# Optimization experiments

Hardware: AMD Instinct MI355X
Metric: run time of the kernel (lower is better)

The kernel has to match this reference:

```python
import jax, jax.numpy as jnp
import numpy as np

KERNEL_MUL = 2.0
KERNEL_NUM = 5
ZERO_SUM_FILL = 100.0  # original replaces zero class-sums with 100 before dividing


def _cal_weight(s_label, t_label):
    # s_label, t_label: [B, C]; normalize each class column by its batch mass,
    # zero out classes absent in either domain (faithful to intended semantics).
    s_sum = jnp.sum(s_label, axis=0, keepdims=True)           # [1, C]
    t_sum = jnp.sum(t_label, axis=0, keepdims=True)           # [1, C]
    s_vec = s_label / jnp.where(s_sum == 0, ZERO_SUM_FILL, s_sum)
    t_vec = t_label / jnp.where(t_sum == 0, ZERO_SUM_FILL, t_sum)
    valid = ((s_sum != 0) & (t_sum != 0)).astype(s_label.dtype)  # [1, C]
    s_vec = s_vec * valid
    t_vec = t_vec * valid
    w_ss = s_vec @ s_vec.T   # [B, B]
    w_tt = t_vec @ t_vec.T   # [B, B]
    w_st = s_vec @ t_vec.T   # [B, B]
    return w_ss, w_tt, w_st


def _multi_kernel(source, target):
    n = source.shape[0] + target.shape[0]
    total = jnp.concatenate([source, target], axis=0)          # [N, D]
    # pairwise squared L2 via GEMM trick: same math as (x_i - x_j)^2 summed over D
    sq = jnp.sum(total * total, axis=1)                        # [N]
    l2 = sq[:, None] + sq[None, :] - 2.0 * (total @ total.T)   # [N, N]
    # bandwidth from detached distances (median-like heuristic)
    bw = jax.lax.stop_gradient(jnp.sum(l2)) / (n * n - n)
    bw = bw / (KERNEL_MUL ** (KERNEL_NUM // 2))
    kernels = jnp.zeros_like(l2)
    for i in range(KERNEL_NUM):
        kernels = kernels + jnp.exp(-l2 / (bw * (KERNEL_MUL ** i)))
    return kernels


def setup_inputs() -> dict:
    key = jax.random.key(0)
    k1, k2, k3, k4 = jax.random.split(key, 4)
    B, D, C = 4096, 256, 31
    return {
        "source": jax.random.normal(k1, (B, D), dtype=jnp.float32),
        "target": jax.random.normal(k2, (B, D), dtype=jnp.float32),
        "s_label": jax.random.uniform(k3, (B, C), dtype=jnp.float32),
        "t_label": jax.random.uniform(k4, (B, C), dtype=jnp.float32),
    }


def reference(source, target, s_label, t_label):
    B = source.shape[0]
    # weights are computed in numpy in the original -> constants w.r.t. grads
    w_ss, w_tt, w_st = _cal_weight(jax.lax.stop_gradient(s_label),
                                   jax.lax.stop_gradient(t_label))
    kernels = _multi_kernel(source, target)                    # [2B, 2B]
    SS = kernels[:B, :B]
    TT = kernels[B:, B:]
    ST = kernels[:B, B:]
    loss = jnp.sum(w_ss * SS + w_tt * TT - 2.0 * w_st * ST)
    return loss.reshape(1)
```

## Files before the change

### kernel.cpp

```cpp
#include <hip/hip_runtime.h>
#include <hip/hip_bf16.h>
#include <math.h>

#define BN 4096
#define DD 256
#define CC 31
#define KP 352
#define AUGA 256
#define AUGB 288
#define LABK 320

typedef __attribute__((ext_vector_type(8))) short bf16x8;
typedef __attribute__((ext_vector_type(4))) float f32x4;

static __device__ inline unsigned short f2bf(float v) {
  __hip_bfloat16 h = __float2bfloat16(v);
  union { __hip_bfloat16 h; unsigned short u; } cv;
  cv.h = h;
  return cv.u;
}
static __device__ inline float bf2f(unsigned short u) {
  return __uint_as_float(((unsigned int)u) << 16);
}


__global__ void colscale_kernel(const float* __restrict__ s_label,
                                const float* __restrict__ t_label,
                                float* __restrict__ aScale,
                                float* __restrict__ bScale) {
  int c = blockIdx.x;
  int t = threadIdx.x;
  double ss = 0.0, ts = 0.0;
  if (c < CC) {
    for (int r = t; r < BN; r += 256) {
      ss += (double)s_label[(size_t)r * CC + c];
      ts += (double)t_label[(size_t)r * CC + c];
    }
  }
  for (int off = 32; off; off >>= 1) {
    ss += __shfl_xor(ss, off);
    ts += __shfl_xor(ts, off);
  }
  __shared__ double rS[4], rT[4];
  int w = t >> 6, lane = t & 63;
  if (lane == 0) { rS[w] = ss; rT[w] = ts; }
  __syncthreads();
  if (t == 0) {
    double s_sum = rS[0] + rS[1] + rS[2] + rS[3];
    double t_sum = rT[0] + rT[1] + rT[2] + rT[3];
    bool valid = (c < CC) && (s_sum != 0.0) && (t_sum != 0.0);
    aScale[c] = valid ? (float)(1.0 / s_sum) : 0.f;
    bScale[c] = valid ? (float)(1.0 / t_sum) : 0.f;
  }
}

__global__ void stats_kernel(const float* __restrict__ source,
                             const float* __restrict__ target,
                             double* __restrict__ colsum,
                             double* __restrict__ sumsq) {
  const int d = threadIdx.x;
  const int r0 = blockIdx.x * 32;
  float cs = 0.f, sq = 0.f;
  for (int r = r0; r < r0 + 32; ++r) {
    const float v = (r < BN) ? source[(size_t)r * DD + d]
                             : target[(size_t)(r - BN) * DD + d];
    cs += v;
    sq += v * v;
  }
  atomicAdd(&colsum[d], (double)cs);
  __shared__ float red[256];
  red[d] = sq;
  __syncthreads();
  for (int s = 128; s; s >>= 1) {
    if (d < s) red[d] += red[d + s];
    __syncthreads();
  }
  if (d == 0) atomicAdd(sumsq, (double)red[0]);
}

__global__ void bw_kernel(const double* __restrict__ sumsq,
                          const double* __restrict__ colsum,
                          float* __restrict__ negc) {
  __shared__ double red[256];
  int t = threadIdx.x;
  double cs = colsum[t];
  red[t] = cs * cs;
  __syncthreads();
  for (int s = 128; s; s >>= 1) {
    if (t < s) red[t] += red[t + s];
    __syncthreads();
  }
  if (t == 0) {
    double suml2 = 2.0 * 8192.0 * (*sumsq) - 2.0 * red[0];
    double bw = suml2 / (8192.0 * 8192.0 - 8192.0);
    bw = bw / 4.0;
    for (int k = 0; k < 5; ++k)
      negc[k] = (float)(-1.0 / (bw * (double)(1 << k)));
  }
}

__global__ void pack_kernel(const float* __restrict__ source,
                            const float* __restrict__ target,
                            const float* __restrict__ s_label,
                            const float* __restrict__ t_label,
                            const float* __restrict__ aScale,
                            const float* __restrict__ bScale,
                            unsigned short* __restrict__ pack) {
  const int vr = blockIdx.x;
  const int l = threadIdx.x;
  const bool isS = (vr < BN);
  const float* xp = isS ? (source + (size_t)vr * DD)
                        : (target + (size_t)(vr - BN) * DD);
  float4 v = ((const float4*)xp)[l];
  unsigned short ub[4] = {f2bf(v.x), f2bf(v.y), f2bf(v.z), f2bf(v.w)};
  float f[4];
#pragma unroll
  for (int e = 0; e < 4; ++e) f[e] = bf2f(ub[e]);
  float sq = f[0] * f[0] + f[1] * f[1] + f[2] * f[2] + f[3] * f[3];
#pragma unroll
  for (int off = 32; off; off >>= 1) sq += __shfl_xor(sq, off);

  const size_t rb = (size_t)vr * KP;
  *(short4*)&pack[rb + l * 4] =
      make_short4((short)ub[0], (short)ub[1], (short)ub[2], (short)ub[3]);

  if (l < 8) {
    const unsigned short one = f2bf(1.0f);
    const float hs = -0.5f * sq;
    const unsigned short hh = f2bf(hs);
    const unsigned short lo = f2bf(hs - bf2f(hh));
    const int c0 = l * 4;
    unsigned short a_aug[4], b_aug[4], labv[4];
#pragma unroll
    for (int e = 0; e < 4; ++e) {
      const int c = c0 + e;
      a_aug[e] = (c == 0) ? hh : (c == 1) ? lo : (c <= 3) ? one : (unsigned short)0;
      b_aug[e] = (c <= 1) ? one : (c == 2) ? hh : (c == 3) ? lo : (unsigned short)0;
      float lv = 0.f;
      if (c < CC) {
        lv = isS ? s_label[(size_t)vr * CC + c] * aScale[c]
                 : t_label[(size_t)(vr - BN) * CC + c] * bScale[c];
      }
      labv[e] = f2bf(lv);
    }
    *(short4*)&pack[rb + AUGA + c0] = make_short4(
        (short)a_aug[0], (short)a_aug[1], (short)a_aug[2], (short)a_aug[3]);
    *(short4*)&pack[rb + AUGB + c0] = make_short4(
        (short)b_aug[0], (short)b_aug[1], (short)b_aug[2], (short)b_aug[3]);
    *(short4*)&pack[rb + LABK + c0] = make_short4(
        (short)labv[0], (short)labv[1], (short)labv[2], (short)labv[3]);
  }
}

__global__ __launch_bounds__(256) void lmmd_main(
    const unsigned short* __restrict__ pack, const float* __restrict__ negc,
    double* __restrict__ accOut) {
  __shared__ __align__(16) unsigned short bufB[2][128][32];
  __shared__ double dred[256];

  const int t = threadIdx.x;
  const int lane = t & 63;
  const int wv = t >> 6;
  const int bi = blockIdx.x >> 6;
  const int bj = blockIdx.x & 63;
  const int r15 = lane & 15;
  const int kb0 = (lane >> 4) * 8;

  const int rowSi = (bi * 64 + wv * 16 + r15) * KP;
  const int rowTi = rowSi + BN * KP;

  const int srow = t >> 1;
  const int soff = (t & 1) * 16;
  const int srowG = (srow < 64) ? (bj * 64 + srow) : (BN + bj * 64 + (srow - 64));
  const size_t sbase = (size_t)srowG * KP;

  constexpr int koAarr[10] = {0, 32, 64, 96, 128, 160, 192, 224, AUGA, LABK};
  constexpr int koBarr[10] = {0, 32, 64, 96, 128, 160, 192, 224, AUGB, LABK};

  f32x4 aSS[4], aTT[4], aST[4], wSS[4], wTT[4], wST[4];
#pragma unroll
  for (int n = 0; n < 4; ++n) {
    aSS[n] = {0.f, 0.f, 0.f, 0.f};
    aTT[n] = {0.f, 0.f, 0.f, 0.f};
    aST[n] = {0.f, 0.f, 0.f, 0.f};
    wSS[n] = {0.f, 0.f, 0.f, 0.f};
    wTT[n] = {0.f, 0.f, 0.f, 0.f};
    wST[n] = {0.f, 0.f, 0.f, 0.f};
  }

  {
    const float4 v0 = *(const float4*)&pack[sbase + koBarr[0] + soff];
    const float4 v1 = *(const float4*)&pack[sbase + koBarr[0] + soff + 8];
    *(float4*)&bufB[0][srow][soff] = v0;
    *(float4*)&bufB[0][srow][soff + 8] = v1;
  }

#pragma unroll
  for (int c = 0; c < 10; ++c) {
    __syncthreads();
    float4 s0, s1;
    if (c < 9) {
      s0 = *(const float4*)&pack[sbase + koBarr[c + 1] + soff];
      s1 = *(const float4*)&pack[sbase + koBarr[c + 1] + soff + 8];
    }
    const bf16x8 aS = *(const bf16x8*)&pack[rowSi + koAarr[c] + kb0];
    const bf16x8 aT = *(const bf16x8*)&pack[rowTi + koAarr[c] + kb0];
    const int cb = c & 1;
#pragma unroll
    for (int n = 0; n < 4; ++n) {
      const bf16x8 bS = *(const bf16x8*)&bufB[cb][n * 16 + r15][kb0];
      const bf16x8 bT = *(const bf16x8*)&bufB[cb][64 + n * 16 + r15][kb0];
      if (c < 9) {
        aSS[n] = __builtin_amdgcn_mfma_f32_16x16x32_bf16(aS, bS, aSS[n], 0, 0, 0);
        aTT[n] = __builtin_amdgcn_mfma_f32_16x16x32_bf16(aT, bT, aTT[n], 0, 0, 0);
        aST[n] = __builtin_amdgcn_mfma_f32_16x16x32_bf16(aS, bT, aST[n], 0, 0, 0);
      } else {
        wSS[n] = __builtin_amdgcn_mfma_f32_16x16x32_bf16(aS, bS, wSS[n], 0, 0, 0);
        wTT[n] = __builtin_amdgcn_mfma_f32_16x16x32_bf16(aT, bT, wTT[n], 0, 0, 0);
        wST[n] = __builtin_amdgcn_mfma_f32_16x16x32_bf16(aS, bT, wST[n], 0, 0, 0);
      }
    }
    if (c < 9) {
      const int nb = (c + 1) & 1;
      *(float4*)&bufB[nb][srow][soff] = s0;
      *(float4*)&bufB[nb][srow][soff + 8] = s1;
    }
  }

  const float nc0 = negc[0], nc1 = negc[1], nc2 = negc[2], nc3 = negc[3],
              nc4 = negc[4];
  double tsum = 0.0;
#pragma unroll
  for (int n = 0; n < 4; ++n) {
#pragma unroll
    for (int e = 0; e < 4; ++e) {
      const float l2ss = -2.f * aSS[n][e];
      const float l2tt = -2.f * aTT[n][e];
      const float l2st = -2.f * aST[n][e];
      const float Kss = __expf(l2ss * nc0) + __expf(l2ss * nc1) +
                        __expf(l2ss * nc2) + __expf(l2ss * nc3) +
                        __expf(l2ss * nc4);
      const float Ktt = __expf(l2tt * nc0) + __expf(l2tt * nc1) +
                        __expf(l2tt * nc2) + __expf(l2tt * nc3) +
                        __expf(l2tt * nc4);
      const float Kst = __expf(l2st * nc0) + __expf(l2st * nc1) +
                        __expf(l2st * nc2) + __expf(l2st * nc3) +
                        __expf(l2st * nc4);
      tsum += (double)(wSS[n][e] * Kss + wTT[n][e] * Ktt -
                       2.f * wST[n][e] * Kst);
    }
  }
  dred[t] = tsum;
  __syncthreads();
  for (int s = 128; s; s >>= 1) {
    if (t < s) dred[t] += dred[t + s];
    __syncthreads();
  }
  if (t == 0) atomicAdd(accOut, dred[0]);
}

__global__ void finalize_kernel(const double* __restrict__ acc,
                                float* __restrict__ out) {
  out[0] = (float)acc[0];
}

extern "C" void kernel_launch(void* const* d_in, const int* in_sizes, int n_in,
                              void* d_out, int out_size, void* d_ws,
                              size_t ws_size, hipStream_t stream) {
  const float* source = (const float*)d_in[0];
  const float* target = (const float*)d_in[1];
  const float* s_label = (const float*)d_in[2];
  const float* t_label = (const float*)d_in[3];

  double* acc = (double*)d_ws;
  double* sumsq = acc + 1;
  double* colsum = acc + 2;
  float* fbase = (float*)((char*)d_ws + 2112);
  float* aScale = fbase;
  float* bScale = fbase + 32;
  float* negc = fbase + 64;
  unsigned short* pack = (unsigned short*)((char*)d_ws + 4096);

  hipMemsetAsync(d_ws, 0, 2112, stream);
  colscale_kernel<<<32, 256, 0, stream>>>(s_label, t_label, aScale, bScale);
  stats_kernel<<<256, 256, 0, stream>>>(source, target, colsum, sumsq);
  bw_kernel<<<1, 256, 0, stream>>>(sumsq, colsum, negc);
  pack_kernel<<<8192, 64, 0, stream>>>(source, target, s_label, t_label,
                                       aScale, bScale, pack);
  lmmd_main<<<4096, 256, 0, stream>>>(pack, negc, acc);
  finalize_kernel<<<1, 1, 0, stream>>>(acc, (float*)d_out);
}
```

Before: 171.4 us.

## Fuse label column sums into stats kernel, merge scale setup, pad LDS rows

Removes the separate colscale kernel by folding the label column sums into the stats kernel through double atomics, and merges the scale computation into the bandwidth kernel. That drops one launch and a poorly coalesced column-strided pass. The pack kernel now handles four rows per 256-thread block instead of one row per 64-thread block. The LDS B buffer row stride is padded from 32 to 40 shorts to reduce bank conflicts in the main kernel. The main kernel's indexing (not shown) must match the new stride.

```diff
diff --git a/kernel.cpp b/kernel.cpp
--- a/kernel.cpp
+++ b/kernel.cpp
@@ -9,6 +9,7 @@
 #define AUGA 256
 #define AUGB 288
 #define LABK 320
+#define LROW 40
 
 typedef __attribute__((ext_vector_type(8))) short bf16x8;
 typedef __attribute__((ext_vector_type(4))) float f32x4;
@@ -24,40 +25,14 @@
 }
 
 
-__global__ void colscale_kernel(const float* __restrict__ s_label,
-                                const float* __restrict__ t_label,
-                                float* __restrict__ aScale,
-                                float* __restrict__ bScale) {
-  int c = blockIdx.x;
-  int t = threadIdx.x;
-  double ss = 0.0, ts = 0.0;
-  if (c < CC) {
-    for (int r = t; r < BN; r += 256) {
-      ss += (double)s_label[(size_t)r * CC + c];
-      ts += (double)t_label[(size_t)r * CC + c];
-    }
-  }
-  for (int off = 32; off; off >>= 1) {
-    ss += __shfl_xor(ss, off);
-    ts += __shfl_xor(ts, off);
-  }
-  __shared__ double rS[4], rT[4];
-  int w = t >> 6, lane = t & 63;
-  if (lane == 0) { rS[w] = ss; rT[w] = ts; }
-  __syncthreads();
-  if (t == 0) {
-    double s_sum = rS[0] + rS[1] + rS[2] + rS[3];
-    double t_sum = rT[0] + rT[1] + rT[2] + rT[3];
-    bool valid = (c < CC) && (s_sum != 0.0) && (t_sum != 0.0);
-    aScale[c] = valid ? (float)(1.0 / s_sum) : 0.f;
-    bScale[c] = valid ? (float)(1.0 / t_sum) : 0.f;
-  }
-}
-
 __global__ void stats_kernel(const float* __restrict__ source,
                              const float* __restrict__ target,
+                             const float* __restrict__ s_label,
+                             const float* __restrict__ t_label,
                              double* __restrict__ colsum,
-                             double* __restrict__ sumsq) {
+                             double* __restrict__ sumsq,
+                             double* __restrict__ labsumS,
+                             double* __restrict__ labsumT) {
   const int d = threadIdx.x;
   const int r0 = blockIdx.x * 32;
   float cs = 0.f, sq = 0.f;
@@ -76,11 +51,24 @@
     __syncthreads();
   }
   if (d == 0) atomicAdd(sumsq, (double)red[0]);
-}
-
-__global__ void bw_kernel(const double* __restrict__ sumsq,
-                          const double* __restrict__ colsum,
-                          float* __restrict__ negc) {
+
+  if (d < CC) {
+    const bool isS = (blockIdx.x < 128);
+    const int lr0 = (isS ? blockIdx.x : blockIdx.x - 128) * 32;
+    const float* lab = isS ? s_label : t_label;
+    float ls = 0.f;
+    for (int r = lr0; r < lr0 + 32; ++r) ls += lab[(size_t)r * CC + d];
+    atomicAdd(isS ? &labsumS[d] : &labsumT[d], (double)ls);
+  }
+}
+
+__global__ void bw_scale_kernel(const double* __restrict__ sumsq,
+                                const double* __restrict__ colsum,
+                                const double* __restrict__ labsumS,
+                                const double* __restrict__ labsumT,
+                                float* __restrict__ negc,
+                                float* __restrict__ aScale,
+                                float* __restrict__ bScale) {
   __shared__ double red[256];
   int t = threadIdx.x;
   double cs = colsum[t];
@@ -97,6 +85,13 @@
     for (int k = 0; k < 5; ++k)
       negc[k] = (float)(-1.0 / (bw * (double)(1 << k)));
   }
+  if (t < 32) {
+    double s_sum = (t < CC) ? labsumS[t] : 0.0;
+    double t_sum = (t < CC) ? labsumT[t] : 0.0;
+    bool valid = (t < CC) && (s_sum != 0.0) && (t_sum != 0.0);
+    aScale[t] = valid ? (float)(1.0 / s_sum) : 0.f;
+    bScale[t] = valid ? (float)(1.0 / t_sum) : 0.f;
+  }
 }
 
 __global__ void pack_kernel(const float* __restrict__ source,
@@ -106,8 +101,8 @@
                             const float* __restrict__ aScale,
                             const float* __restrict__ bScale,
                             unsigned short* __restrict__ pack) {
-  const int vr = blockIdx.x;
-  const int l = threadIdx.x;
+  const int vr = blockIdx.x * 4 + (threadIdx.x >> 6);
+  const int l = threadIdx.x & 63;
   const bool isS = (vr < BN);
   const float* xp = isS ? (source + (size_t)vr * DD)
                         : (target + (size_t)(vr - BN) * DD);
@@ -155,7 +150,7 @@
 __global__ __launch_bounds__(256) void lmmd_main(
     const unsigned short* __restrict__ pack, const float* __restrict__ negc,
     double* __restrict__ accOut) {
-  __shared__ __align__(16) unsigned short bufB[2][128][32];
+  __shared__ __align__(16) unsigned short bufB[2][128][LROW];
   __shared__ double dred[256];
 
   const int t = threadIdx.x;
@@ -275,18 +270,21 @@
   double* acc = (double*)d_ws;
   double* sumsq = acc + 1;
   double* colsum = acc + 2;
-  float* fbase = (float*)((char*)d_ws + 2112);
+  double* labsumS = acc + 258;
+  double* labsumT = acc + 290;
+  float* fbase = (float*)((char*)d_ws + 2624);
   float* aScale = fbase;
   float* bScale = fbase + 32;
   float* negc = fbase + 64;
   unsigned short* pack = (unsigned short*)((char*)d_ws + 4096);
 
-  hipMemsetAsync(d_ws, 0, 2112, stream);
-  colscale_kernel<<<32, 256, 0, stream>>>(s_label, t_label, aScale, bScale);
-  stats_kernel<<<256, 256, 0, stream>>>(source, target, colsum, sumsq);
-  bw_kernel<<<1, 256, 0, stream>>>(sumsq, colsum, negc);
-  pack_kernel<<<8192, 64, 0, stream>>>(source, target, s_label, t_label,
-                                       aScale, bScale, pack);
+  hipMemsetAsync(d_ws, 0, 2624, stream);
+  stats_kernel<<<256, 256, 0, stream>>>(source, target, s_label, t_label,
+                                        colsum, sumsq, labsumS, labsumT);
+  bw_scale_kernel<<<1, 256, 0, stream>>>(sumsq, colsum, labsumS, labsumT,
+                                         negc, aScale, bScale);
+  pack_kernel<<<2048, 256, 0, stream>>>(source, target, s_label, t_label,
+                                        aScale, bScale, pack);
   lmmd_main<<<4096, 256, 0, stream>>>(pack, negc, acc);
   finalize_kernel<<<1, 1, 0, stream>>>(acc, (float*)d_out);
 }
```

New measurement: 166.2 us. -3.0%, faster.
